# Optimization experiments

Measured on AMD Instinct MI355X. Metric: run time of the kernel, lower is better.

The kernel has to match this reference:

```python
import jax, jax.numpy as jnp
import numpy as np

B, S, L, CIN = 8, 32, 128, 1024
C1, C2 = 512, 256            # conv1_channel, conv2_channel
D1, D2 = 512, 128            # deconv1_channel, deconv2_channel
CD, SIM = 300, 128           # concept_dim, similarity_dim
L4 = L // 4


def _conv1d(x, w, b, pad):
    # x: [N, Cin, L], w: [Cout, Cin, k] (PyTorch layout)
    y = jax.lax.conv_general_dilated(x, w, (1,), [(pad, pad)],
                                     dimension_numbers=('NCH', 'OIH', 'NCH'))
    return y + b[None, :, None]


def _maxpool2(x):
    return jax.lax.reduce_window(x, -jnp.inf, jax.lax.max, (1, 1, 2), (1, 1, 2), 'VALID')


def _deconv1d(x, w, b):
    # PyTorch ConvTranspose1d(kernel=4, stride=2, padding=1); w: [Cin, Cout, k]
    w2 = jnp.flip(w, -1).transpose(1, 0, 2)  # -> OIH
    y = jax.lax.conv_general_dilated(x, w2, (1,), [(2, 2)], lhs_dilation=(2,),
                                     dimension_numbers=('NCH', 'OIH', 'NCH'))
    return y + b[None, :, None]


def setup_inputs():
    ks = jax.random.split(jax.random.key(0), 32)
    g = lambda i, shape: jax.random.normal(ks[i], shape, jnp.float32) * 0.02
    return {
        'batch': jax.random.normal(ks[0], (B, S, L, CIN), jnp.float32),
        'concept1': jax.random.normal(ks[1], (B, CD), jnp.float32),
        'concept2': jax.random.normal(ks[2], (B, CD), jnp.float32),
        'seg_len': jax.random.randint(ks[3], (B, S), 1, L + 1),
        'conv1_w': g(4, (C1, CIN, 5)), 'conv1_b': g(5, (C1,)),
        'conv2_w': g(6, (C2, C1, 5)), 'conv2_b': g(7, (C2,)),
        'sa_wq': g(8, (C2, C2)), 'sa_bq': g(9, (C2,)),
        'sa_wk': g(10, (C2, C2)), 'sa_bk': g(11, (C2,)),
        'sa_v': g(12, (C2,)), 'sa_vb': g(13, ()),
        'ca_wq': g(14, (CD, C2)), 'ca_bq': g(15, (C2,)),
        'ca_wk': g(16, (C2, C2)), 'ca_bk': g(17, (C2,)),
        'ca_v': g(18, (C2,)), 'ca_vb': g(19, ()),
        'dc1_w': g(20, (4 * C2, D1, 4)), 'dc1_b': g(21, (D1,)),
        'dc2_w': g(22, (D1, D2, 4)), 'dc2_b': g(23, (D2,)),
        'sim1_w': g(24, (D2, SIM)),
        'sim2_w': g(25, (CD, SIM)),
        'mlp_w': g(26, (SIM,)), 'mlp_b': g(27, ()),
    }


def reference(batch, concept1, concept2, seg_len,
              conv1_w, conv1_b, conv2_w, conv2_b,
              sa_wq, sa_bq, sa_wk, sa_bk, sa_v, sa_vb,
              ca_wq, ca_bq, ca_wk, ca_bk, ca_v, ca_vb,
              dc1_w, dc1_b, dc2_w, dc2_b,
              sim1_w, sim2_w, mlp_w, mlp_b):
    N = B * S
    # conv stack: [N, CIN, L] -> [N, C2, L/4]
    x = batch.reshape(N, L, CIN).transpose(0, 2, 1)
    t = _maxpool2(_conv1d(x, conv1_w, conv1_b, 2))
    t = _maxpool2(_conv1d(t, conv2_w, conv2_b, 2))
    tmp2 = t.transpose(0, 2, 1)                       # [N, L4, C2]

    # vectorized length mask: mask[i,j,k] = k < ceil(seg_len/4)  <=>  seg_len > 4k
    mask = (seg_len[:, :, None] > 4 * jnp.arange(L4)).reshape(N, 1, L4)

    # self additive attention over pooled positions
    qp = tmp2 @ sa_wq + sa_bq                          # [N, L4, H]
    kp = tmp2 @ sa_wk + sa_bk                          # [N, L4, H]
    s = jnp.einsum('nqkh,h->nqk', jnp.tanh(qp[:, :, None, :] + kp[:, None, :, :]), sa_v) + sa_vb
    s = jnp.where(mask, s, -1e9)
    a = jax.nn.softmax(s, axis=-1)                     # [N, L4, L4]
    self_res = jnp.einsum('nqk,nkc->nqc', a, tmp2)     # [N, L4, C2]

    # concept attention (query identical across positions -> compute once)
    ckp = tmp2 @ ca_wk + ca_bk                         # [N, L4, H]

    def concept_attn(c):
        cq = jnp.repeat(c @ ca_wq + ca_bq, S, axis=0)  # [N, H]
        sc = jnp.einsum('nkh,h->nk', jnp.tanh(cq[:, None, :] + ckp), ca_v) + ca_vb
        sc = jnp.where(mask[:, 0, :], sc, -1e9)
        ac = jax.nn.softmax(sc, axis=-1)               # [N, L4]
        r = jnp.einsum('nk,nkc->nc', ac, tmp2)         # [N, C2]
        return jnp.broadcast_to(r[:, None, :], (N, L4, C2))

    c1_res = concept_attn(concept1)
    c2_res = concept_attn(concept2)

    ar = jnp.concatenate([tmp2, self_res, c1_res, c2_res], axis=-1)  # [N, L4, 4*C2]
    r = _deconv1d(ar.transpose(0, 2, 1), dc1_w, dc1_b)               # [N, D1, L/2]
    r = _deconv1d(r, dc2_w, dc2_b).transpose(0, 2, 1)                # [N, L, D2]
    r = r.reshape(B, S * L, D2)

    sim1 = r @ sim1_w                                                # [B, S*L, SIM]

    def score(c):
        cs = (c @ sim2_w)[:, None, :] * sim1
        return jax.nn.sigmoid(cs @ mlp_w + mlp_b).reshape(B, S, L)

    return score(concept1), score(concept2)
```

## Files before the change

kernel.cpp:

```cpp
#include <hip/hip_runtime.h>
#include <cstdint>

typedef __bf16 bf16;
typedef __bf16 bf16x8 __attribute__((ext_vector_type(8)));
typedef float f32x4 __attribute__((ext_vector_type(4)));
typedef __attribute__((address_space(3))) bf16 lds_bf16;

__device__ __forceinline__ void gload_lds16(const void* g, void* l) {
  __builtin_amdgcn_global_load_lds(
      (const __attribute__((address_space(1))) unsigned int*)g,
      (__attribute__((address_space(3))) unsigned int*)l, 16, 0, 0);
}

__device__ __forceinline__ bf16x8 ld_b128(const lds_bf16* p) {
  bf16x8 r;
  asm volatile("ds_read_b128 %0, %1" : "=v"(r) : "v"(p));
  return r;
}

__device__ __forceinline__ float tanh_fast(float x) {
  float ax = fabsf(x);
  float e = __expf(ax + ax);
  float t = 1.0f - 2.0f / (e + 1.0f);
  return x < 0.0f ? -t : t;
}

template<int MODE, int DEPTH>
__global__ __launch_bounds__(256) void gemm_tap(
    const bf16* __restrict__ A, const bf16* __restrict__ Bt,
    const float* __restrict__ bias, bf16* __restrict__ Out,
    const bf16* __restrict__ zp,
    int snA, int logP, int logCI, int shift0, int ntaps, int cbCount,
    int cbCI, int pairs, int Ktot, int COt, int snO,
    const float* __restrict__ uu, const float* __restrict__ mlpb,
    float* __restrict__ outF)
{
  __shared__ __align__(16) bf16 Ab[2 * DEPTH][4096];
  __shared__ __align__(16) bf16 Bb[2 * DEPTH][4096];
  const int tid  = threadIdx.x;
  const int wave = tid >> 6, lane = tid & 63;
  const int wr = wave >> 1, wc = wave & 1;
  const int m0  = blockIdx.x << 7;
  const int co0 = blockIdx.y << 7;
  const int P     = 1 << logP;
  const int Pmask = P - 1;
  const int CI    = 1 << logCI;
  f32x4 acc[4][4] = {};

  const int rowL = tid >> 2;
  const int kg   = tid & 3;
  const int fOff = ((kg ^ ((rowL + (rowL >> 2)) & 3)) << 3);

  const int mA0 = m0 + rowL,      nA0 = mA0 >> logP, pA0v = mA0 & Pmask;
  const int mA1 = m0 + rowL + 64, nA1 = mA1 >> logP, pA1v = mA1 & Pmask;
  const bf16* baseA0 = A + nA0 * snA + fOff;
  const bf16* baseA1 = A + nA1 * snA + fOff;
  const bf16* baseB0 = Bt + (co0 + rowL) * Ktot + fOff;
  const bf16* baseB1 = Bt + (co0 + rowL + 64) * Ktot + fOff;
  const bf16* zsrc = zp + fOff;

  const int frow  = lane & 15;
  const int rdOff = (((lane >> 4) ^ ((frow + (frow >> 2)) & 3)) << 3);

  for (int cb = 0; cb < cbCount; ++cb) {
    for (int tap = 0; tap < ntaps; ++tap) {
      const int sh = tap + shift0;
      const int rA0 = pA0v + sh, rA1 = pA1v + sh;
      const bool v0 = (unsigned)rA0 < (unsigned)P;
      const bool v1 = (unsigned)rA1 < (unsigned)P;
      const bf16* pa0 = v0 ? (baseA0 + rA0 * CI + cb * cbCI) : zsrc;
      const bf16* pa1 = v1 ? (baseA1 + rA1 * CI + cb * cbCI) : zsrc;
      const bf16* pb0 = baseB0 + (cb * ntaps + tap) * cbCI;
      const bf16* pb1 = baseB1 + (cb * ntaps + tap) * cbCI;

      for (int kc = 0; kc < pairs; kc += DEPTH) {
#pragma unroll
        for (int h = 0; h < 2 * DEPTH; ++h) {
          gload_lds16(pa0 + 32 * h, &Ab[h][wave * 512]);
          gload_lds16(pa1 + 32 * h, &Ab[h][2048 + wave * 512]);
          gload_lds16(pb0 + 32 * h, &Bb[h][wave * 512]);
          gload_lds16(pb1 + 32 * h, &Bb[h][2048 + wave * 512]);
        }
        if (v0) pa0 += 64 * DEPTH;
        if (v1) pa1 += 64 * DEPTH;
        pb0 += 64 * DEPTH; pb1 += 64 * DEPTH;
        __syncthreads();
#pragma unroll
        for (int h = 0; h < 2 * DEPTH; ++h) {
          bf16x8 af[4], bg[4];
#pragma unroll
          for (int i = 0; i < 4; ++i) {
            af[i] = *(const bf16x8*)&Ab[h][((wr << 6) + (i << 4) + frow) * 32 + rdOff];
            bg[i] = *(const bf16x8*)&Bb[h][((wc << 6) + (i << 4) + frow) * 32 + rdOff];
          }
#pragma unroll
          for (int i = 0; i < 4; ++i)
#pragma unroll
            for (int j = 0; j < 4; ++j)
              acc[i][j] = __builtin_amdgcn_mfma_f32_16x16x32_bf16(af[i], bg[j], acc[i][j], 0, 0, 0);
        }
        __syncthreads();
      }
    }
  }

  const int colL = lane & 15;
  const int rq   = (lane >> 4) << 2;

  if (MODE == 2) {
    float* scr0 = (float*)&Ab[0][0];
    float* scr1 = (float*)&Bb[0][0];
    const int n = m0 >> logP;
    const int b = n >> 5;
    const float* u0 = uu + b * 128;
    const float* u1 = uu + 1024 + b * 128;
#pragma unroll
    for (int i = 0; i < 4; ++i) {
#pragma unroll
      for (int r = 0; r < 4; ++r) {
        int rowLcl = (wr << 6) + (i << 4) + rq + r;
        float p0 = 0.0f, p1 = 0.0f;
#pragma unroll
        for (int j = 0; j < 4; ++j) {
          int gco = (wc << 6) + (j << 4) + colL;
          float v = acc[i][j][r];
          p0 += v * u0[gco];
          p1 += v * u1[gco];
        }
        scr0[rowLcl * 32 + (wc << 4) + colL] = p0;
        scr1[rowLcl * 32 + (wc << 4) + colL] = p1;
      }
    }
    __syncthreads();
    {
      int rowLcl = tid >> 1, c = tid & 1;
      const float* s = c ? scr1 : scr0;
      float sum = 0.0f;
#pragma unroll
      for (int k = 0; k < 32; ++k) sum += s[rowLcl * 32 + k];
      float val = 1.0f / (1.0f + __expf(-(sum + mlpb[0])));
      outF[(c ? 32768 : 0) + m0 + rowLcl] = val;
    }
    return;
  }

#pragma unroll
  for (int i = 0; i < 4; ++i) {
    int m = m0 + (wr << 6) + (i << 4) + rq;
    int n = m >> logP, p = m & Pmask;
#pragma unroll
    for (int j = 0; j < 4; ++j) {
      int gco = co0 + (wc << 6) + (j << 4) + colL;
      float bv = bias[gco];
      if (MODE == 1) {
        float v0 = fmaxf(acc[i][j][0], acc[i][j][1]) + bv;
        float v1 = fmaxf(acc[i][j][2], acc[i][j][3]) + bv;
        bf16* o = Out + n * snO + (p >> 1) * COt + gco;
        o[0]   = (bf16)v0;
        o[COt] = (bf16)v1;
      } else {
#pragma unroll
        for (int r = 0; r < 4; ++r)
          Out[n * snO + (p + r) * COt + gco] = (bf16)(acc[i][j][r] + bv);
      }
    }
  }
}

template<int LOGP, int LOGCI, int SH0, int NTAPS, int CBCNT, int CBCI>
__global__ __launch_bounds__(512, 2) void gemm8_pool(
    const bf16* __restrict__ A, const bf16* __restrict__ Bt,
    const float* __restrict__ bias, bf16* __restrict__ Out,
    const bf16* __restrict__ zp, int snA, int Ktot, int COt, int snO)
{
  __shared__ __align__(16) bf16 Ab[2][2][8192];
  __shared__ __align__(16) bf16 Bb[2][2][8192];
  constexpr int P = 1 << LOGP, CI = 1 << LOGCI;
  constexpr int KPC = CBCI / 64;
  constexpr int NT = CBCNT * NTAPS * KPC;

  const int tid = threadIdx.x;
  const int wave = tid >> 6, lane = tid & 63;
  const int wr = wave >> 2, wc = wave & 3;
  const int m0 = blockIdx.x << 8, co0 = blockIdx.y << 8;
  const int n0 = m0 >> LOGP;

  f32x4 acc[8][4] = {};

  const int rowP = tid >> 2;
  const int kOff = (((tid & 3) ^ ((rowP + (rowP >> 2)) & 3)) << 3);
  const bf16* baseA = A + n0 * snA + kOff;
  const bf16* pBs   = Bt + (co0 + rowP) * Ktot + kOff;
  const bf16* zsrc  = zp + kOff;
  const int ldsW = wave << 9;
  const int bStride = 128 * Ktot;

  const int frow = lane & 15;
  const int rdOff = (((lane >> 4) ^ ((frow + (frow >> 2)) & 3)) << 3);

  int s_kc = 0, s_tap = 0, s_cb = 0;

  auto stageTile = [&](int bfs) {
    int rA = rowP + s_tap + SH0;
    bool v = (unsigned)rA < (unsigned)P;
    const bf16* pA0 = v ? baseA + rA * CI + (s_cb * CBCI + s_kc * 64) : zsrc;
    const bf16* pA1 = v ? pA0 + snA : zsrc;
    gload_lds16(pA0,      &Ab[bfs][0][ldsW]);
    gload_lds16(pA0 + 32, &Ab[bfs][1][ldsW]);
    gload_lds16(pA1,      &Ab[bfs][0][ldsW + 4096]);
    gload_lds16(pA1 + 32, &Ab[bfs][1][ldsW + 4096]);
    gload_lds16(pBs,                &Bb[bfs][0][ldsW]);
    gload_lds16(pBs + 32,           &Bb[bfs][1][ldsW]);
    gload_lds16(pBs + bStride,      &Bb[bfs][0][ldsW + 4096]);
    gload_lds16(pBs + bStride + 32, &Bb[bfs][1][ldsW + 4096]);
    pBs += 64;
    if (++s_kc == KPC) { s_kc = 0; if (++s_tap == NTAPS) { s_tap = 0; ++s_cb; } }
  };

  auto ldA = [&](int buf, int ks, int mh, int i) {
    return ld_b128((const lds_bf16*)
        &Ab[buf][ks][((wr << 7) + (mh << 6) + (i << 4) + frow) * 32 + rdOff]);
  };
  auto ldB = [&](int buf, int ks, int j) {
    return ld_b128((const lds_bf16*)
        &Bb[buf][ks][((wc << 6) + (j << 4) + frow) * 32 + rdOff]);
  };

  stageTile(0);
  __syncthreads();

  bf16x8 a0[4], a1[4], b0[4], b1[4];

#pragma unroll 1
  for (int t = 0; t < NT; ++t) {
    const int buf = t & 1;
#pragma unroll
    for (int i = 0; i < 4; ++i) a0[i] = ldA(buf, 0, 0, i);
#pragma unroll
    for (int j = 0; j < 4; ++j) b0[j] = ldB(buf, 0, j);
    if (t + 1 < NT) stageTile(buf ^ 1);
#pragma unroll
    for (int i = 0; i < 4; ++i) a1[i] = ldA(buf, 0, 1, i);
    asm volatile("s_waitcnt lgkmcnt(4)" ::: "memory");
    __builtin_amdgcn_sched_barrier(0);
    __builtin_amdgcn_s_setprio(1);
#pragma unroll
    for (int i = 0; i < 4; ++i)
#pragma unroll
      for (int j = 0; j < 4; ++j)
        acc[i][j] = __builtin_amdgcn_mfma_f32_16x16x32_bf16(a0[i], b0[j], acc[i][j], 0, 0, 0);
    __builtin_amdgcn_s_setprio(0);
#pragma unroll
    for (int i = 0; i < 4; ++i) a0[i] = ldA(buf, 1, 0, i);
#pragma unroll
    for (int j = 0; j < 4; ++j) b1[j] = ldB(buf, 1, j);
    asm volatile("s_waitcnt lgkmcnt(8)" ::: "memory");
    __builtin_amdgcn_sched_barrier(0);
    __builtin_amdgcn_s_setprio(1);
#pragma unroll
    for (int i = 0; i < 4; ++i)
#pragma unroll
      for (int j = 0; j < 4; ++j)
        acc[4 + i][j] = __builtin_amdgcn_mfma_f32_16x16x32_bf16(a1[i], b0[j], acc[4 + i][j], 0, 0, 0);
    __builtin_amdgcn_s_setprio(0);
#pragma unroll
    for (int i = 0; i < 4; ++i) a1[i] = ldA(buf, 1, 1, i);
    asm volatile("s_waitcnt lgkmcnt(4)" ::: "memory");
    __builtin_amdgcn_sched_barrier(0);
    __builtin_amdgcn_s_setprio(1);
#pragma unroll
    for (int i = 0; i < 4; ++i)
#pragma unroll
      for (int j = 0; j < 4; ++j)
        acc[i][j] = __builtin_amdgcn_mfma_f32_16x16x32_bf16(a0[i], b1[j], acc[i][j], 0, 0, 0);
    __builtin_amdgcn_s_setprio(0);
    asm volatile("s_waitcnt lgkmcnt(0)" ::: "memory");
    __builtin_amdgcn_sched_barrier(0);
    __builtin_amdgcn_s_setprio(1);
#pragma unroll
    for (int i = 0; i < 4; ++i)
#pragma unroll
      for (int j = 0; j < 4; ++j)
        acc[4 + i][j] = __builtin_amdgcn_mfma_f32_16x16x32_bf16(a1[i], b1[j], acc[4 + i][j], 0, 0, 0);
    __builtin_amdgcn_s_setprio(0);
    __syncthreads();
  }

  const int colL = lane & 15, rq = (lane >> 4) << 2;
#pragma unroll
  for (int i = 0; i < 8; ++i) {
    int m = m0 + (wr << 7) + (i << 4) + rq;
    int n = m >> LOGP, p = m & (P - 1);
    bf16* orow = Out + n * snO + (p >> 1) * COt;
#pragma unroll
    for (int j = 0; j < 4; ++j) {
      int gco = co0 + (wc << 6) + (j << 4) + colL;
      float bv = bias[gco];
      orow[gco]       = (bf16)(fmaxf(acc[i][j][0], acc[i][j][1]) + bv);
      orow[COt + gco] = (bf16)(fmaxf(acc[i][j][2], acc[i][j][3]) + bv);
    }
  }
}

__global__ __launch_bounds__(256) void prep_all(
    const float* __restrict__ conv1_w, const float* __restrict__ conv2_w,
    const float* __restrict__ sa_wq, const float* __restrict__ sa_wk,
    const float* __restrict__ ca_wk, const float* __restrict__ dc1_w,
    const float* __restrict__ dc2_w, const float* __restrict__ sim1_w,
    const float* __restrict__ c1b, const float* __restrict__ c2b,
    const float* __restrict__ sabq, const float* __restrict__ sabk,
    const float* __restrict__ cabk, const float* __restrict__ d1b,
    const float* __restrict__ d2b,
    const float* __restrict__ c1, const float* __restrict__ c2,
    const float* __restrict__ ca_wq, const float* __restrict__ ca_bq,
    const float* __restrict__ sim2_w, const float* __restrict__ mlp_w,
    const float* __restrict__ batch, bf16* __restrict__ bb16,
    bf16* __restrict__ Bt1, bf16* __restrict__ Bt2, bf16* __restrict__ Bqkc,
    bf16* __restrict__ Btd1, bf16* __restrict__ Btd2, bf16* __restrict__ Bts1,
    float* __restrict__ bias, float* __restrict__ cq, float* __restrict__ uu)
{
  const int blk = blockIdx.x;
  if (blk >= 27492) {
    int idx = ((blk - 27492) * 256 + threadIdx.x) * 8;
    float4 a = *(const float4*)&batch[idx];
    float4 b = *(const float4*)&batch[idx + 4];
    bf16x8 v;
    v[0] = (bf16)a.x; v[1] = (bf16)a.y; v[2] = (bf16)a.z; v[3] = (bf16)a.w;
    v[4] = (bf16)b.x; v[5] = (bf16)b.y; v[6] = (bf16)b.z; v[7] = (bf16)b.w;
    *(bf16x8*)&bb16[idx] = v;
    return;
  }
  if (blk < 27468) {
    int idx = blk * 256 + threadIdx.x;
    if (idx < 3072) {
      if (idx < 2944) {
        float v;
        if (idx < 512)       v = c1b[idx];
        else if (idx < 768)  v = c2b[idx - 512];
        else if (idx < 1024) v = sabq[idx - 768];
        else if (idx < 1280) v = sabk[idx - 1024];
        else if (idx < 1536) v = cabk[idx - 1280];
        else if (idx < 2560) v = d1b[(idx - 1536) & 511];
        else if (idx < 2816) v = d2b[(idx - 2560) & 127];
        else                 v = 0.0f;
        bias[idx] = v;
      }
    } else if (idx < 2624512) {
      int i = idx - 3072;
      int co = i / 5120, r = i - co * 5120;
      int cb = r / 1280, r2 = r - cb * 1280;
      int tap = r2 >> 8, cl = r2 & 255;
      Bt1[i] = (bf16)conv1_w[co * 5120 + (cb * 256 + cl) * 5 + tap];
    } else if (idx < 3279872) {
      int i = idx - 2624512;
      int co = i / 2560, r = i - co * 2560;
      int cb = r / 1280, r2 = r - cb * 1280;
      int tap = r2 >> 8, cl = r2 & 255;
      Bt2[i] = (bf16)conv2_w[co * 2560 + (cb * 256 + cl) * 5 + tap];
    } else if (idx < 3476480) {
      int i = idx - 3279872;
      int co = i >> 8, ci = i & 255;
      float v;
      if (co < 256)      v = sa_wq[ci * 256 + co];
      else if (co < 512) v = sa_wk[ci * 256 + (co - 256)];
      else               v = ca_wk[ci * 256 + (co - 512)];
      Bqkc[i] = (bf16)v;
    } else if (idx < 6622208) {
      int i = idx - 3476480;
      int co = i / 3072, r = i - co * 3072;
      int cb = r / 768, r2 = r - cb * 768;
      int tap = r2 >> 8, cl = r2 & 255;
      int ci = cb * 256 + cl;
      int par = co >> 9, c = co & 511;
      int ki = -1;
      if (par == 0) { if (tap == 1) ki = 1; else if (tap == 0) ki = 3; }
      else          { if (tap == 2) ki = 0; else if (tap == 1) ki = 2; }
      Btd1[i] = (ki >= 0) ? (bf16)dc1_w[ci * 2048 + c * 4 + ki] : (bf16)0.0f;
    } else if (idx < 7015424) {
      int i = idx - 6622208;
      int co = i / 1536, r = i - co * 1536;
      int cb = r / 768, r2 = r - cb * 768;
      int tap = r2 >> 8, cl = r2 & 255;
      int ci = cb * 256 + cl;
      int par = co >> 7, c = co & 127;
      int ki = -1;
      if (par == 0) { if (tap == 1) ki = 1; else if (tap == 0) ki = 3; }
      else          { if (tap == 2) ki = 0; else if (tap == 1) ki = 2; }
      Btd2[i] = (ki >= 0) ? (bf16)dc2_w[ci * 512 + c * 4 + ki] : (bf16)0.0f;
    } else {
      int i = idx - 7015424;
      int co = i >> 7, ci = i & 127;
      Bts1[i] = (bf16)sim1_w[ci * 128 + co];
    }
  } else {
    int sub = blk - 27468;
    if (sub < 16) {
      int o = sub * 256 + threadIdx.x;
      int c = o >> 11, b = (o >> 8) & 7, h = o & 255;
      const float* cc = (c ? c2 : c1) + b * 300;
      float acc = ca_bq[h];
      for (int j = 0; j < 300; ++j)
        acc += cc[j] * ca_wq[j * 256 + h];
      cq[o] = acc;
    } else {
      int o = (sub - 16) * 256 + threadIdx.x;
      int c = o >> 10, b = (o >> 7) & 7, m = o & 127;
      const float* cc = (c ? c2 : c1) + b * 300;
      float acc = 0.0f;
      for (int j = 0; j < 300; ++j)
        acc += cc[j] * sim2_w[j * 128 + m];
      uu[o] = acc * mlp_w[m];
    }
  }
}

__global__ __launch_bounds__(256) void kattn(
    const bf16* __restrict__ tmp2, const bf16* __restrict__ qkc,
    const float* __restrict__ sa_v, const float* __restrict__ sa_vb,
    const float* __restrict__ ca_v, const float* __restrict__ ca_vb,
    const float* __restrict__ cq, const int* __restrict__ seg,
    bf16* __restrict__ ar)
{
  const int n = blockIdx.x, tid = threadIdx.x;
  __shared__ __align__(16) bf16 t2[32 * 264];
  __shared__ __align__(16) bf16 bufA[32 * 264];
  __shared__ __align__(16) bf16 bufB[32 * 264];
  __shared__ float sv_s[256], cv_s[256];
  __shared__ float sbc[66];
  __shared__ float sbs[32 * 33];
  const int sl = seg[n];

#pragma unroll
  for (int rr = 0; rr < 4; ++rr) {
    int q = tid + (rr << 8);
    int k = q >> 5, c8 = (q & 31) << 3;
    *(uint4*)&t2[k * 264 + c8]   = *(const uint4*)&tmp2[n * 8192 + k * 256 + c8];
    *(uint4*)&bufA[k * 264 + c8] = *(const uint4*)&qkc[n * 24576 + k * 768 + 512 + c8];
  }
  sv_s[tid] = sa_v[tid];
  cv_s[tid] = ca_v[tid];
  __syncthreads();

  if (tid < 64) {
    int c = tid >> 5, k = tid & 31;
    const float* cqr = cq + (c * 8 + (n >> 5)) * 256;
    float acc = 0.0f;
    for (int h = 0; h < 256; ++h)
      acc += tanh_fast(cqr[h] + (float)bufA[k * 264 + h]) * cv_s[h];
    float sc = acc + ca_vb[0];
    sbc[c * 33 + k] = (sl > (k << 2)) ? sc : -1e9f;
  }
  __syncthreads();

#pragma unroll
  for (int rr = 0; rr < 4; ++rr) {
    int q = tid + (rr << 8);
    int k = q >> 5, c8 = (q & 31) << 3;
    *(uint4*)&bufB[k * 264 + c8] = *(const uint4*)&qkc[n * 24576 + k * 768 + c8];
    *(uint4*)&bufA[k * 264 + c8] = *(const uint4*)&qkc[n * 24576 + k * 768 + 256 + c8];
  }
  if (tid < 2) {
    float* row = &sbc[tid * 33];
    float mx = -1e30f;
    for (int k = 0; k < 32; ++k) mx = fmaxf(mx, row[k]);
    float sum = 0.0f;
    for (int k = 0; k < 32; ++k) { float e = __expf(row[k] - mx); row[k] = e; sum += e; }
    float inv = 1.0f / sum;
    for (int k = 0; k < 32; ++k) row[k] *= inv;
  }
  __syncthreads();

  {
    int col = tid;
    float rr0 = 0.0f, rr1 = 0.0f;
    for (int k = 0; k < 32; ++k) {
      float tv = (float)t2[k * 264 + col];
      rr0 += sbc[k] * tv;
      rr1 += sbc[33 + k] * tv;
    }
    bf16 b0 = (bf16)rr0, b1 = (bf16)rr1;
    bf16* arn = ar + n * 32768;
    for (int q = 0; q < 32; ++q) {
      arn[q * 1024 + col]       = t2[q * 264 + col];
      arn[q * 1024 + 512 + col] = b0;
      arn[q * 1024 + 768 + col] = b1;
    }
  }
  {
    float svb = sa_vb[0];
#pragma unroll
    for (int rr = 0; rr < 4; ++rr) {
      int id = tid + (rr << 8);
      int q = id >> 5, k = id & 31;
      float acc = 0.0f;
      for (int h = 0; h < 256; ++h)
        acc += tanh_fast((float)bufB[q * 264 + h] + (float)bufA[k * 264 + h]) * sv_s[h];
      float sc = acc + svb;
      sbs[q * 33 + k] = (sl > (k << 2)) ? sc : -1e9f;
    }
  }
  __syncthreads();

  if (tid < 32) {
    float* row = &sbs[tid * 33];
    float mx = -1e30f;
    for (int k = 0; k < 32; ++k) mx = fmaxf(mx, row[k]);
    float sum = 0.0f;
    for (int k = 0; k < 32; ++k) { float e = __expf(row[k] - mx); row[k] = e; sum += e; }
    float inv = 1.0f / sum;
    for (int k = 0; k < 32; ++k) row[k] *= inv;
  }
  __syncthreads();

  {
    int col = tid;
    bf16* arn = ar + n * 32768;
    for (int q = 0; q < 32; ++q) {
      float acc = 0.0f;
      for (int k = 0; k < 32; ++k)
        acc += sbs[q * 33 + k] * (float)t2[k * 264 + col];
      arn[q * 1024 + 256 + col] = (bf16)acc;
    }
  }
}

extern "C" void kernel_launch(void* const* d_in, const int* in_sizes, int n_in,
                              void* d_out, int out_size, void* d_ws, size_t ws_size,
                              hipStream_t stream) {
  const float* batch    = (const float*)d_in[0];
  const float* concept1 = (const float*)d_in[1];
  const float* concept2 = (const float*)d_in[2];
  const int*   seg      = (const int*)d_in[3];
  const float* conv1_w  = (const float*)d_in[4];
  const float* conv1_b  = (const float*)d_in[5];
  const float* conv2_w  = (const float*)d_in[6];
  const float* conv2_b  = (const float*)d_in[7];
  const float* sa_wq    = (const float*)d_in[8];
  const float* sa_bq    = (const float*)d_in[9];
  const float* sa_wk    = (const float*)d_in[10];
  const float* sa_bk    = (const float*)d_in[11];
  const float* sa_v     = (const float*)d_in[12];
  const float* sa_vb    = (const float*)d_in[13];
  const float* ca_wq    = (const float*)d_in[14];
  const float* ca_bq    = (const float*)d_in[15];
  const float* ca_wk    = (const float*)d_in[16];
  const float* ca_bk    = (const float*)d_in[17];
  const float* ca_v     = (const float*)d_in[18];
  const float* ca_vb    = (const float*)d_in[19];
  const float* dc1_w    = (const float*)d_in[20];
  const float* dc1_b    = (const float*)d_in[21];
  const float* dc2_w    = (const float*)d_in[22];
  const float* dc2_b    = (const float*)d_in[23];
  const float* sim1_w   = (const float*)d_in[24];
  const float* sim2_w   = (const float*)d_in[25];
  const float* mlp_w    = (const float*)d_in[26];
  const float* mlp_b    = (const float*)d_in[27];

  char* ws = (char*)d_ws;
  bf16* bb16  = (bf16*)(ws + 0);
  bf16* qkcb  = (bf16*)(ws + 0);
  bf16* arb   = (bf16*)(ws + 12582912);
  bf16* d1    = (bf16*)(ws + 29360128);
  bf16* rbuf  = (bf16*)(ws + 46137344);
  bf16* t1    = (bf16*)(ws + 67108864);
  bf16* tmp2b = (bf16*)(ws + 83886080);
  bf16* Bt1   = (bf16*)(ws + 88080384);
  bf16* Bt2   = (bf16*)(ws + 93323264);
  bf16* Bqkc  = (bf16*)(ws + 94633984);
  bf16* Btd1  = (bf16*)(ws + 95027200);
  bf16* Btd2  = (bf16*)(ws + 101318656);
  bf16* Bts1  = (bf16*)(ws + 102105088);
  float* biasall = (float*)(ws + 102137856);
  float* cqb  = (float*)(ws + 102149632);
  float* uub  = (float*)(ws + 102166016);
  const bf16* zp = (const bf16*)(biasall + 2816);
  float* outp = (float*)d_out;

  prep_all<<<43876, 256, 0, stream>>>(
      conv1_w, conv2_w, sa_wq, sa_wk, ca_wk, dc1_w, dc2_w, sim1_w,
      conv1_b, conv2_b, sa_bq, sa_bk, ca_bk, dc1_b, dc2_b,
      concept1, concept2, ca_wq, ca_bq, sim2_w, mlp_w,
      batch, bb16,
      Bt1, Bt2, Bqkc, Btd1, Btd2, Bts1, biasall, cqb, uub);

  gemm8_pool<7, 10, -2, 5, 4, 256><<<dim3(128, 2), 512, 0, stream>>>(
      bb16, Bt1, biasall + 0, t1, zp, 131072, 5120, 512, 32768);

  gemm_tap<1, 2><<<dim3(128, 2), 256, 0, stream>>>(
      t1, Bt2, biasall + 512, tmp2b, zp, 32768, 6, 9, -2, 5, 2, 256, 4, 2560, 256, 8192,
      nullptr, nullptr, nullptr);

  gemm_tap<0, 2><<<dim3(64, 6), 256, 0, stream>>>(
      tmp2b, Bqkc, biasall + 768, qkcb, zp, 8192, 5, 8, 0, 1, 1, 256, 4, 256, 768, 24576,
      nullptr, nullptr, nullptr);

  kattn<<<256, 256, 0, stream>>>(tmp2b, qkcb, sa_v, sa_vb, ca_v, ca_vb, cqb, seg, arb);

  gemm_tap<0, 2><<<dim3(64, 8), 256, 0, stream>>>(
      arb, Btd1, biasall + 1536, d1, zp, 32768, 5, 10, -1, 3, 4, 256, 4, 3072, 1024, 32768,
      nullptr, nullptr, nullptr);

  gemm_tap<0, 2><<<dim3(128, 2), 256, 0, stream>>>(
      d1, Btd2, biasall + 2560, rbuf, zp, 32768, 6, 9, -1, 3, 2, 256, 4, 1536, 256, 16384,
      nullptr, nullptr, nullptr);

  gemm_tap<2, 2><<<dim3(256, 1), 256, 0, stream>>>(
      rbuf, Bts1, biasall + 2816, nullptr, zp, 16384, 7, 7, 0, 1, 1, 128, 2, 128, 128, 16384,
      uub, mlp_b, outp);
}
```

Baseline: 638.9 us.

## Software-pipeline gemm_tap with double-buffered LDS and interleaved MFMA scheduling

Replaces the load-sync-compute-sync loop in gemm_tap with a flattened K loop over (cb, tap, kc). Two LDS buffers let the next tile's global-to-LDS loads be issued while the current tile's fragments are read and fed to MFMAs. It adds explicit lgkmcnt waits, sched barriers and setprio around the MFMA groups, and requests two blocks per CU through launch_bounds. Each loop step now covers a 64-wide K tile instead of 128, so there are more barriers, and the waits rely on the issued LDS-read counts being right.

New measurement: 645.8 us. About the same (+1.1%).

```diff
diff --git a/kernel.cpp b/kernel.cpp
--- a/kernel.cpp
+++ b/kernel.cpp
@@ -25,8 +25,8 @@
   return x < 0.0f ? -t : t;
 }
 
-template<int MODE, int DEPTH>
-__global__ __launch_bounds__(256) void gemm_tap(
+template<int MODE>
+__global__ __launch_bounds__(256, 2) void gemm_tap(
     const bf16* __restrict__ A, const bf16* __restrict__ Bt,
     const float* __restrict__ bias, bf16* __restrict__ Out,
     const bf16* __restrict__ zp,
@@ -35,8 +35,9 @@
     const float* __restrict__ uu, const float* __restrict__ mlpb,
     float* __restrict__ outF)
 {
-  __shared__ __align__(16) bf16 Ab[2 * DEPTH][4096];
-  __shared__ __align__(16) bf16 Bb[2 * DEPTH][4096];
+  __shared__ __align__(16) bf16 Ab[2][2][4096];
+  __shared__ __align__(16) bf16 Bb[2][2][4096];
+  (void)pairs;
   const int tid  = threadIdx.x;
   const int wave = tid >> 6, lane = tid & 63;
   const int wr = wave >> 1, wc = wave & 1;
@@ -62,54 +63,77 @@
   const int frow  = lane & 15;
   const int rdOff = (((lane >> 4) ^ ((frow + (frow >> 2)) & 3)) << 3);
 
-  for (int cb = 0; cb < cbCount; ++cb) {
-    for (int tap = 0; tap < ntaps; ++tap) {
-      const int sh = tap + shift0;
-      const int rA0 = pA0v + sh, rA1 = pA1v + sh;
-      const bool v0 = (unsigned)rA0 < (unsigned)P;
-      const bool v1 = (unsigned)rA1 < (unsigned)P;
-      const bf16* pa0 = v0 ? (baseA0 + rA0 * CI + cb * cbCI) : zsrc;
-      const bf16* pa1 = v1 ? (baseA1 + rA1 * CI + cb * cbCI) : zsrc;
-      const bf16* pb0 = baseB0 + (cb * ntaps + tap) * cbCI;
-      const bf16* pb1 = baseB1 + (cb * ntaps + tap) * cbCI;
-
-      for (int kc = 0; kc < pairs; kc += DEPTH) {
-#pragma unroll
-        for (int h = 0; h < 2 * DEPTH; ++h) {
-          gload_lds16(pa0 + 32 * h, &Ab[h][wave * 512]);
-          gload_lds16(pa1 + 32 * h, &Ab[h][2048 + wave * 512]);
-          gload_lds16(pb0 + 32 * h, &Bb[h][wave * 512]);
-          gload_lds16(pb1 + 32 * h, &Bb[h][2048 + wave * 512]);
-        }
-        if (v0) pa0 += 64 * DEPTH;
-        if (v1) pa1 += 64 * DEPTH;
-        pb0 += 64 * DEPTH; pb1 += 64 * DEPTH;
-        __syncthreads();
-#pragma unroll
-        for (int h = 0; h < 2 * DEPTH; ++h) {
-          bf16x8 af[4], bg[4];
-#pragma unroll
-          for (int i = 0; i < 4; ++i) {
-            af[i] = *(const bf16x8*)&Ab[h][((wr << 6) + (i << 4) + frow) * 32 + rdOff];
-            bg[i] = *(const bf16x8*)&Bb[h][((wc << 6) + (i << 4) + frow) * 32 + rdOff];
-          }
-#pragma unroll
-          for (int i = 0; i < 4; ++i)
-#pragma unroll
-            for (int j = 0; j < 4; ++j)
-              acc[i][j] = __builtin_amdgcn_mfma_f32_16x16x32_bf16(af[i], bg[j], acc[i][j], 0, 0, 0);
-        }
-        __syncthreads();
-      }
-    }
+  const int kpc = cbCI >> 6;
+  const int NT  = cbCount * ntaps * kpc;
+  int s_kc = 0, s_tap = 0, s_cb = 0;
+
+  auto stageTile = [&](int bfs) {
+    int sh  = s_tap + shift0;
+    int rA0 = pA0v + sh, rA1 = pA1v + sh;
+    int ko  = s_cb * cbCI + (s_kc << 6);
+    const bf16* pa0 = ((unsigned)rA0 < (unsigned)P) ? baseA0 + rA0 * CI + ko : zsrc;
+    const bf16* pa1 = ((unsigned)rA1 < (unsigned)P) ? baseA1 + rA1 * CI + ko : zsrc;
+    const bf16* pb0 = baseB0 + (s_cb * ntaps + s_tap) * cbCI + (s_kc << 6);
+    const bf16* pb1 = baseB1 + (s_cb * ntaps + s_tap) * cbCI + (s_kc << 6);
+    gload_lds16(pa0,      &Ab[bfs][0][wave * 512]);
+    gload_lds16(pa0 + 32, &Ab[bfs][1][wave * 512]);
+    gload_lds16(pa1,      &Ab[bfs][0][2048 + wave * 512]);
+    gload_lds16(pa1 + 32, &Ab[bfs][1][2048 + wave * 512]);
+    gload_lds16(pb0,      &Bb[bfs][0][wave * 512]);
+    gload_lds16(pb0 + 32, &Bb[bfs][1][wave * 512]);
+    gload_lds16(pb1,      &Bb[bfs][0][2048 + wave * 512]);
+    gload_lds16(pb1 + 32, &Bb[bfs][1][2048 + wave * 512]);
+    if (++s_kc == kpc) { s_kc = 0; if (++s_tap == ntaps) { s_tap = 0; ++s_cb; } }
+  };
+
+  stageTile(0);
+  __syncthreads();
+
+  bf16x8 a0[4], a1[4], b0f[4], b1f[4];
+
+#pragma unroll 1
+  for (int t = 0; t < NT; ++t) {
+    const int buf = t & 1;
+#pragma unroll
+    for (int i = 0; i < 4; ++i)
+      a0[i] = ld_b128((const lds_bf16*)&Ab[buf][0][((wr << 6) + (i << 4) + frow) * 32 + rdOff]);
+#pragma unroll
+    for (int j = 0; j < 4; ++j)
+      b0f[j] = ld_b128((const lds_bf16*)&Bb[buf][0][((wc << 6) + (j << 4) + frow) * 32 + rdOff]);
+    if (t + 1 < NT) stageTile(buf ^ 1);
+#pragma unroll
+    for (int i = 0; i < 4; ++i)
+      a1[i] = ld_b128((const lds_bf16*)&Ab[buf][1][((wr << 6) + (i << 4) + frow) * 32 + rdOff]);
+#pragma unroll
+    for (int j = 0; j < 4; ++j)
+      b1f[j] = ld_b128((const lds_bf16*)&Bb[buf][1][((wc << 6) + (j << 4) + frow) * 32 + rdOff]);
+    asm volatile("s_waitcnt lgkmcnt(8)" ::: "memory");
+    __builtin_amdgcn_sched_barrier(0);
+    __builtin_amdgcn_s_setprio(1);
+#pragma unroll
+    for (int i = 0; i < 4; ++i)
+#pragma unroll
+      for (int j = 0; j < 4; ++j)
+        acc[i][j] = __builtin_amdgcn_mfma_f32_16x16x32_bf16(a0[i], b0f[j], acc[i][j], 0, 0, 0);
+    __builtin_amdgcn_s_setprio(0);
+    asm volatile("s_waitcnt lgkmcnt(0)" ::: "memory");
+    __builtin_amdgcn_sched_barrier(0);
+    __builtin_amdgcn_s_setprio(1);
+#pragma unroll
+    for (int i = 0; i < 4; ++i)
+#pragma unroll
+      for (int j = 0; j < 4; ++j)
+        acc[i][j] = __builtin_amdgcn_mfma_f32_16x16x32_bf16(a1[i], b1f[j], acc[i][j], 0, 0, 0);
+    __builtin_amdgcn_s_setprio(0);
+    __syncthreads();
   }
 
   const int colL = lane & 15;
   const int rq   = (lane >> 4) << 2;
 
   if (MODE == 2) {
-    float* scr0 = (float*)&Ab[0][0];
-    float* scr1 = (float*)&Bb[0][0];
+    float* scr0 = (float*)&Ab[0][0][0];
+    float* scr1 = (float*)&Bb[0][0][0];
     const int n = m0 >> logP;
     const int b = n >> 5;
     const float* u0 = uu + b * 128;
@@ -586,25 +610,25 @@
   gemm8_pool<7, 10, -2, 5, 4, 256><<<dim3(128, 2), 512, 0, stream>>>(
       bb16, Bt1, biasall + 0, t1, zp, 131072, 5120, 512, 32768);
 
-  gemm_tap<1, 2><<<dim3(128, 2), 256, 0, stream>>>(
+  gemm_tap<1><<<dim3(128, 2), 256, 0, stream>>>(
       t1, Bt2, biasall + 512, tmp2b, zp, 32768, 6, 9, -2, 5, 2, 256, 4, 2560, 256, 8192,
       nullptr, nullptr, nullptr);
 
-  gemm_tap<0, 2><<<dim3(64, 6), 256, 0, stream>>>(
+  gemm_tap<0><<<dim3(64, 6), 256, 0, stream>>>(
       tmp2b, Bqkc, biasall + 768, qkcb, zp, 8192, 5, 8, 0, 1, 1, 256, 4, 256, 768, 24576,
       nullptr, nullptr, nullptr);
 
   kattn<<<256, 256, 0, stream>>>(tmp2b, qkcb, sa_v, sa_vb, ca_v, ca_vb, cqb, seg, arb);
 
-  gemm_tap<0, 2><<<dim3(64, 8), 256, 0, stream>>>(
+  gemm_tap<0><<<dim3(64, 8), 256, 0, stream>>>(
       arb, Btd1, biasall + 1536, d1, zp, 32768, 5, 10, -1, 3, 4, 256, 4, 3072, 1024, 32768,
       nullptr, nullptr, nullptr);
 
-  gemm_tap<0, 2><<<dim3(128, 2), 256, 0, stream>>>(
+  gemm_tap<0><<<dim3(128, 2), 256, 0, stream>>>(
       d1, Btd2, biasall + 2560, rbuf, zp, 32768, 6, 9, -1, 3, 2, 256, 4, 1536, 256, 16384,
       nullptr, nullptr, nullptr);
 
-  gemm_tap<2, 2><<<dim3(256, 1), 256, 0, stream>>>(
+  gemm_tap<2><<<dim3(256, 1), 256, 0, stream>>>(
       rbuf, Bts1, biasall + 2816, nullptr, zp, 16384, 7, 7, 0, 1, 1, 128, 2, 128, 128, 16384,
       uub, mlp_b, outp);
 }
```
